# Performance work log

Hardware: AMD Instinct MI355X
Metric: run time of the kernel (lower is better)

## Reference

```python
import jax, jax.numpy as jnp
import numpy as np
import math

DIM = 1024
NUM_HEADS = 16
HEAD_DIM = DIM // NUM_HEADS
LOGIT_SCALE_MAX = math.log(1.0 / 0.01)
EPS = 1e-12  # F.normalize eps


def setup_inputs() -> dict:
    key = jax.random.key(0)
    ks = jax.random.split(key, 4)
    L, N, C = 1024, 8, DIM
    scale = HEAD_DIM ** -0.5
    x = jax.random.normal(ks[0], (L, N, C), dtype=jnp.float32)
    in_proj_weight = jax.random.normal(ks[1], (3 * C, C), dtype=jnp.float32) * scale
    in_proj_bias = jnp.zeros((3 * C,), dtype=jnp.float32)
    logit_scale = jnp.full((NUM_HEADS, 1, 1), math.log(10.0), dtype=jnp.float32)
    head_scale = jnp.ones((NUM_HEADS, 1, 1), dtype=jnp.float32)
    out_w = jax.random.normal(ks[2], (C, C), dtype=jnp.float32) * (C ** -0.5)
    out_b = jax.random.normal(ks[3], (C,), dtype=jnp.float32) * 0.01
    return {"x": x, "in_proj_weight": in_proj_weight, "in_proj_bias": in_proj_bias,
            "logit_scale": logit_scale, "head_scale": head_scale,
            "out_w": out_w, "out_b": out_b}


def _l2_normalize(t):
    # matches F.normalize(t, dim=-1): t / max(||t||_2, eps)
    n = jnp.sqrt(jnp.sum(t * t, axis=-1, keepdims=True))
    return t / jnp.maximum(n, EPS)


def reference(x, in_proj_weight, in_proj_bias, logit_scale, head_scale, out_w, out_b):
    L, N, C = x.shape
    H, hd = NUM_HEADS, HEAD_DIM
    qkv = x @ in_proj_weight.T + in_proj_bias          # (L, N, 3C)
    q, k, v = jnp.split(qkv, 3, axis=-1)               # each (L, N, C)

    def to_heads(t):  # (L, N, C) -> (N, H, L, hd)
        return t.reshape(L, N, H, hd).transpose(1, 2, 0, 3)

    q, k, v = to_heads(q), to_heads(k), to_heads(v)
    # scaled-cosine attention
    ls = jnp.exp(jnp.minimum(logit_scale, LOGIT_SCALE_MAX))  # (H,1,1) broadcasts
    attn = jnp.einsum('nhld,nhmd->nhlm', _l2_normalize(q), _l2_normalize(k)) * ls
    attn = jax.nn.softmax(attn, axis=-1)               # (N, H, L, L)
    o = jnp.einsum('nhlm,nhmd->nhld', attn, v)         # (N, H, L, hd)
    o = o * head_scale                                  # per-head scale
    o = o.transpose(2, 0, 1, 3).reshape(L, N, C)       # back to (L, N, C)
    return o @ out_w.T + out_b
```

## Files before the change

kernel.cpp:

```cpp
#include <hip/hip_runtime.h>
#include <hip/hip_bf16.h>

typedef __hip_bfloat16 bf16;
typedef __attribute__((ext_vector_type(8))) short bf16x8;
typedef __attribute__((ext_vector_type(4))) float f32x4;

#define LOGIT_MAX 4.6051702f

__device__ __forceinline__ float4 load4(const float* p) { return *(const float4*)p; }

__device__ __forceinline__ void store4bf(bf16* p, float4 v) {
    union { bf16 b[4]; uint2 u; } t;
    t.b[0] = __float2bfloat16(v.x); t.b[1] = __float2bfloat16(v.y);
    t.b[2] = __float2bfloat16(v.z); t.b[3] = __float2bfloat16(v.w);
    *(uint2*)p = t.u;
}

__device__ __forceinline__ void async16(const bf16* g, const bf16* lds) {
    __builtin_amdgcn_global_load_lds(
        (const __attribute__((address_space(1))) void*)g,
        (__attribute__((address_space(3))) void*)lds, 16, 0, 0);
}

__global__ __launch_bounds__(256) void prep_kernel(
    const void* __restrict__ x, const void* __restrict__ w_in, const void* __restrict__ out_w,
    const void* __restrict__ b_in, const void* __restrict__ out_b,
    const void* __restrict__ ls, const void* __restrict__ hs,
    bf16* __restrict__ xb, bf16* __restrict__ wb, bf16* __restrict__ owb,
    float* __restrict__ smallf, int* __restrict__ flag)
{
    __shared__ int cnt;
    if (threadIdx.x == 0) cnt = 0;
    __syncthreads();
    {
        const unsigned short* xs = (const unsigned short*)x;
        int c = 0;
        for (int i = threadIdx.x; i < 4096; i += 256) {
            const unsigned e = (xs[i] >> 7) & 0xFF;
            if (e >= 0x90) c++;
        }
        atomicAdd(&cnt, c);
    }
    __syncthreads();
    const int f = (cnt > 64) ? 1 : 0;

    if (blockIdx.x == 0) {
        if (threadIdx.x == 0) *flag = f;
        for (int idx = threadIdx.x; idx < 4128; idx += 256) {
            float v;
            if (f) {
                if (idx < 3072)      v = ((const float*)b_in)[idx];
                else if (idx < 4096) v = ((const float*)out_b)[idx - 3072];
                else if (idx < 4112) v = expf(fminf(((const float*)ls)[idx - 4096], LOGIT_MAX));
                else                 v = ((const float*)hs)[idx - 4112];
            } else {
                if (idx < 3072)      v = __bfloat162float(((const bf16*)b_in)[idx]);
                else if (idx < 4096) v = __bfloat162float(((const bf16*)out_b)[idx - 3072]);
                else if (idx < 4112) v = expf(fminf(__bfloat162float(((const bf16*)ls)[idx - 4096]), LOGIT_MAX));
                else                 v = __bfloat162float(((const bf16*)hs)[idx - 4112]);
            }
            smallf[idx] = v;
        }
    }
    if (f != 1) return;
    const size_t NX = 8388608, NW = 3145728, NO = 1048576;
    const size_t t0   = ((size_t)blockIdx.x * 256 + threadIdx.x) * 4;
    const size_t step = (size_t)gridDim.x * 256 * 4;
    for (size_t i = t0; i < NX; i += step) store4bf(xb + i, load4((const float*)x + i));
    for (size_t i = t0; i < NW; i += step) store4bf(wb + i, load4((const float*)w_in + i));
    for (size_t i = t0; i < NO; i += step) store4bf(owb + i, load4((const float*)out_w + i));
}

__global__ __launch_bounds__(256, 3) void qkv_gemm_mfma_kernel(
    const int* __restrict__ flag,
    const bf16* __restrict__ Xws, const bf16* __restrict__ Wws,
    const bf16* __restrict__ Xdir, const bf16* __restrict__ Wdir,
    const float* __restrict__ bias_f,
    bf16* __restrict__ q, bf16* __restrict__ k, bf16* __restrict__ vt)
{
    const bf16* X = (*flag) ? Xws : Xdir;
    const bf16* W = (*flag) ? Wws : Wdir;
    __shared__ bf16 A_lds[128 * 64];
    __shared__ bf16 B_lds[128 * 64];
    const int tid  = threadIdx.x;
    const int w    = tid >> 6;
    const int lane = tid & 63;
    const int l16  = lane & 15, quad = lane >> 4;
    const int wm   = w >> 1, wn = w & 1;
    const int row0 = blockIdx.y * 128;
    const int col0 = blockIdx.x * 128;
    const int sr   = lane >> 3, sc = lane & 7;
    const int scg  = sc ^ sr;

    f32x4 acc[4][4] = {};

    for (int kt = 0; kt < 1024; kt += 64) {
        __syncthreads();
#pragma unroll
        for (int i = 0; i < 4; i++) {
            const int br = w * 32 + i * 8;
            async16(X + (size_t)(row0 + br + sr) * 1024 + kt + scg * 8, &A_lds[br * 64]);
            async16(W + (size_t)(col0 + br + sr) * 1024 + kt + scg * 8, &B_lds[br * 64]);
        }
        __syncthreads();

#pragma unroll
        for (int kh = 0; kh < 2; kh++) {
            bf16x8 af[4], bf[4];
#pragma unroll
            for (int mt = 0; mt < 4; mt++) {
                const int row = wm * 64 + mt * 16 + l16;
                af[mt] = *(const bf16x8*)&A_lds[row * 64 + (((quad + kh * 4) ^ (row & 7)) * 8)];
            }
#pragma unroll
            for (int nt = 0; nt < 4; nt++) {
                const int row = wn * 64 + nt * 16 + l16;
                bf[nt] = *(const bf16x8*)&B_lds[row * 64 + (((quad + kh * 4) ^ (row & 7)) * 8)];
            }
#pragma unroll
            for (int mt = 0; mt < 4; mt++)
#pragma unroll
                for (int nt = 0; nt < 4; nt++)
                    acc[mt][nt] = __builtin_amdgcn_mfma_f32_16x16x32_bf16(af[mt], bf[nt], acc[mt][nt], 0, 0, 0);
        }
    }

    const int cbase = col0 + wn * 64;
    const int part  = cbase >> 10;
    const int h     = (cbase & 1023) >> 6;
    float bias[4];
#pragma unroll
    for (int nt = 0; nt < 4; nt++) bias[nt] = bias_f[cbase + nt * 16 + l16];

    if (part < 2) {
        bf16* dst0 = (part == 0) ? q : k;
#pragma unroll
        for (int mt = 0; mt < 4; mt++) {
#pragma unroll
            for (int rg = 0; rg < 4; rg++) {
                const int r = row0 + wm * 64 + mt * 16 + quad * 4 + rg;
                const int l = r >> 3, nn = r & 7;
                float val[4]; float ss = 0.f;
#pragma unroll
                for (int nt = 0; nt < 4; nt++) {
                    val[nt] = acc[mt][nt][rg] + bias[nt];
                    ss += val[nt] * val[nt];
                }
                ss += __shfl_xor(ss, 1); ss += __shfl_xor(ss, 2);
                ss += __shfl_xor(ss, 4); ss += __shfl_xor(ss, 8);
                const float inv = 1.f / fmaxf(sqrtf(ss), 1e-12f);
                bf16* dp = dst0 + ((size_t)((nn * 16 + h) * 1024 + l)) * 64;
#pragma unroll
                for (int nt = 0; nt < 4; nt++)
                    dp[nt * 16 + l16] = __float2bfloat16(val[nt] * inv);
            }
        }
    } else {
#pragma unroll
        for (int mt = 0; mt < 4; mt++) {
#pragma unroll
            for (int rg = 0; rg < 4; rg++) {
                const int r = row0 + wm * 64 + mt * 16 + quad * 4 + rg;
                const int l = r >> 3, nn = r & 7;
#pragma unroll
                for (int nt = 0; nt < 4; nt++) {
                    const int d = nt * 16 + l16;
                    vt[((size_t)((nn * 16 + h) * 64 + d)) * 1024 + l] =
                        __float2bfloat16(acc[mt][nt][rg] + bias[nt]);
                }
            }
        }
    }
}

__global__ __launch_bounds__(512, 2) void attn_mfma_kernel(
    const bf16* __restrict__ q, const bf16* __restrict__ k,
    const bf16* __restrict__ vt, const float* __restrict__ scale_f,
    bf16* __restrict__ o)
{
    __shared__ bf16 K_lds[64][64];
    __shared__ bf16 Vt_lds[64][64];
    __shared__ bf16 P_lds[8][32][72];
    __shared__ float l_lds[8][32];

    const int bid  = blockIdx.x;
    const int qt   = bid >> 7;
    const int nh   = bid & 127;
    const int h    = nh & 15;
    const int n    = nh >> 4;
    const int tid  = threadIdx.x;
    const int w    = tid >> 6;
    const int lane = tid & 63;
    const int l16  = lane & 15;
    const int quad = lane >> 4;

    const size_t base = (size_t)nh * (1024 * 64);
    const float ls   = scale_f[4096 + h];
    const float hs   = scale_f[4112 + h];
    const float lsl2 = ls * 1.4426950408889634f;

    bf16x8 qf[2][2];
#pragma unroll
    for (int u = 0; u < 2; u++) {
        const int qrow = qt * 256 + w * 32 + u * 16 + l16;
        const bf16* qp = q + base + (size_t)qrow * 64 + quad * 8;
        qf[u][0] = *(const bf16x8*)qp;
        qf[u][1] = *(const bf16x8*)(qp + 32);
    }

    f32x4 o_acc[2][4] = {};
    float l_part[2] = {0.f, 0.f};

    const int sr = lane >> 3;
    const int sc = lane & 7;

    for (int j0 = 0; j0 < 1024; j0 += 64) {
        __syncthreads();
        {
            const int row = w * 8 + sr;
            const int cg  = sc ^ (row & 7);
            async16(k  + base + (size_t)(j0 + row) * 64 + cg * 8, &K_lds[w * 8][0]);
            async16(vt + base + (size_t)row * 1024 + j0 + cg * 8, &Vt_lds[w * 8][0]);
        }
        __syncthreads();

        f32x4 s8[2][4];
#pragma unroll
        for (int s = 0; s < 4; s++) {
            const int krow = s * 16 + l16;
            const int swz  = krow & 7;
            const bf16x8 kf0 = *(const bf16x8*)&K_lds[krow][(quad ^ swz) * 8];
            const bf16x8 kf1 = *(const bf16x8*)&K_lds[krow][((quad + 4) ^ swz) * 8];
#pragma unroll
            for (int u = 0; u < 2; u++) {
                f32x4 a = {};
                a = __builtin_amdgcn_mfma_f32_16x16x32_bf16(kf0, qf[u][0], a, 0, 0, 0);
                a = __builtin_amdgcn_mfma_f32_16x16x32_bf16(kf1, qf[u][1], a, 0, 0, 0);
                s8[u][s] = a;
            }
        }

#pragma unroll
        for (int u = 0; u < 2; u++) {
#pragma unroll
            for (int s = 0; s < 4; s++) {
                union { bf16 b[4]; uint2 uu; } pk;
                float sum = 0.f;
#pragma unroll
                for (int r = 0; r < 4; r++) {
                    const float p = exp2f(fmaf(s8[u][s][r], lsl2, -lsl2));
                    pk.b[r] = __float2bfloat16(p);
                    sum += p;
                }
                l_part[u] += sum;
                *(uint2*)&P_lds[w][u * 16 + l16][s * 16 + quad * 4] = pk.uu;
            }
        }

        bf16x8 pf[2][2];
#pragma unroll
        for (int u = 0; u < 2; u++) {
            pf[u][0] = *(const bf16x8*)&P_lds[w][u * 16 + l16][quad * 8];
            pf[u][1] = *(const bf16x8*)&P_lds[w][u * 16 + l16][32 + quad * 8];
        }
#pragma unroll
        for (int ds = 0; ds < 4; ds++) {
            const int vrow = ds * 16 + l16;
            const int swz  = vrow & 7;
            const bf16x8 vf0 = *(const bf16x8*)&Vt_lds[vrow][(quad ^ swz) * 8];
            const bf16x8 vf1 = *(const bf16x8*)&Vt_lds[vrow][((quad + 4) ^ swz) * 8];
#pragma unroll
            for (int u = 0; u < 2; u++) {
                o_acc[u][ds] = __builtin_amdgcn_mfma_f32_16x16x32_bf16(pf[u][0], vf0, o_acc[u][ds], 0, 0, 0);
                o_acc[u][ds] = __builtin_amdgcn_mfma_f32_16x16x32_bf16(pf[u][1], vf1, o_acc[u][ds], 0, 0, 0);
            }
        }
    }

#pragma unroll
    for (int u = 0; u < 2; u++) {
        float v = l_part[u];
        v += __shfl_xor(v, 16);
        v += __shfl_xor(v, 32);
        l_lds[w][u * 16 + l16] = v;
    }

#pragma unroll
    for (int u = 0; u < 2; u++) {
#pragma unroll
        for (int r = 0; r < 4; r++) {
            const float inv = hs / l_lds[w][u * 16 + quad * 4 + r];
            const int row_l = qt * 256 + w * 32 + u * 16 + quad * 4 + r;
            bf16* dst = o + ((size_t)row_l * 8 + n) * 1024 + h * 64 + l16;
#pragma unroll
            for (int ds = 0; ds < 4; ds++)
                dst[ds * 16] = __float2bfloat16(o_acc[u][ds][r] * inv);
        }
    }
}

__global__ __launch_bounds__(256, 3) void out_gemm_mfma_kernel(
    const int* __restrict__ flag,
    const bf16* __restrict__ A,
    const bf16* __restrict__ Bws, const bf16* __restrict__ Bdir,
    const float* __restrict__ bias_f,
    float* __restrict__ outf, bf16* __restrict__ outb)
{
    const int f = *flag;
    const bf16* B = f ? Bws : Bdir;
    __shared__ bf16 A_lds[128 * 64];
    __shared__ bf16 B_lds[128 * 64];
    const int tid  = threadIdx.x;
    const int w    = tid >> 6;
    const int lane = tid & 63;
    const int l16  = lane & 15, quad = lane >> 4;
    const int wm   = w >> 1, wn = w & 1;
    const int row0 = blockIdx.y * 128;
    const int col0 = blockIdx.x * 128;
    const int sr   = lane >> 3, sc = lane & 7;
    const int scg  = sc ^ sr;

    f32x4 acc[4][4] = {};

    for (int kt = 0; kt < 1024; kt += 64) {
        __syncthreads();
#pragma unroll
        for (int i = 0; i < 4; i++) {
            const int br = w * 32 + i * 8;
            async16(A + (size_t)(row0 + br + sr) * 1024 + kt + scg * 8, &A_lds[br * 64]);
            async16(B + (size_t)(col0 + br + sr) * 1024 + kt + scg * 8, &B_lds[br * 64]);
        }
        __syncthreads();

#pragma unroll
        for (int kh = 0; kh < 2; kh++) {
            bf16x8 af[4], bf[4];
#pragma unroll
            for (int mt = 0; mt < 4; mt++) {
                const int row = wm * 64 + mt * 16 + l16;
                af[mt] = *(const bf16x8*)&A_lds[row * 64 + (((quad + kh * 4) ^ (row & 7)) * 8)];
            }
#pragma unroll
            for (int nt = 0; nt < 4; nt++) {
                const int row = wn * 64 + nt * 16 + l16;
                bf[nt] = *(const bf16x8*)&B_lds[row * 64 + (((quad + kh * 4) ^ (row & 7)) * 8)];
            }
#pragma unroll
            for (int mt = 0; mt < 4; mt++)
#pragma unroll
                for (int nt = 0; nt < 4; nt++)
                    acc[mt][nt] = __builtin_amdgcn_mfma_f32_16x16x32_bf16(af[mt], bf[nt], acc[mt][nt], 0, 0, 0);
        }
    }

#pragma unroll
    for (int mt = 0; mt < 4; mt++) {
        const int rbase = row0 + wm * 64 + mt * 16 + quad * 4;
#pragma unroll
        for (int nt = 0; nt < 4; nt++) {
            const int c = col0 + wn * 64 + nt * 16 + l16;
            const float bias = bias_f[c];
#pragma unroll
            for (int rg = 0; rg < 4; rg++) {
                const float v = acc[mt][nt][rg] + bias;
                const size_t idx = (size_t)(rbase + rg) * 1024 + c;
                if (f) outf[idx] = v; else outb[idx] = __float2bfloat16(v);
            }
        }
    }
}

extern "C" void kernel_launch(void* const* d_in, const int* in_sizes, int n_in,
                              void* d_out, int out_size, void* d_ws, size_t ws_size,
                              hipStream_t stream)
{
    const size_t SEG = (size_t)8 * 16 * 1024 * 64;
    bf16* qn  = (bf16*)d_ws;
    bf16* kn  = qn + SEG;
    bf16* vt  = kn + SEG;
    bf16* ow  = vt + SEG;
    bf16* xb  = ow + SEG;
    bf16* wb  = xb + SEG;
    bf16* owb = wb + 3145728;
    float* smallf = (float*)(owb + 1048576);
    int*   flag   = (int*)(smallf + 4128);

    prep_kernel<<<4096, 256, 0, stream>>>(
        d_in[0], d_in[1], d_in[5], d_in[2], d_in[6], d_in[3], d_in[4],
        xb, wb, owb, smallf, flag);

    qkv_gemm_mfma_kernel<<<dim3(3072 / 128, 8192 / 128), 256, 0, stream>>>(
        flag, xb, wb, (const bf16*)d_in[0], (const bf16*)d_in[1], smallf, qn, kn, vt);

    attn_mfma_kernel<<<dim3(128 * 4), 512, 0, stream>>>(qn, kn, vt, smallf, ow);

    out_gemm_mfma_kernel<<<dim3(1024 / 128, 8192 / 128), 256, 0, stream>>>(
        flag, ow, owb, (const bf16*)d_in[5], smallf + 3072,
        (float*)d_out, (bf16*)d_out);
}
```

Baseline: 288.0 us.

## Fuse all stages into one persistent cooperative kernel with grid syncs

Replaces the four kernel launches (prep, QKV GEMM, attention, output GEMM) with one cooperative kernel that walks each stage's tiles in grid-stride fashion and separates stages with grid.sync. The attention stage now uses 256-thread blocks covering 128 queries instead of 512 threads covering 256, and the grid is capped at 512 blocks based on occupancy. This is meant to remove launch gaps and tail effects between kernels, at the cost of grid-wide barriers, a fixed persistent grid, shared-memory reuse across stages, and possibly lower per-stage occupancy.

```diff
diff --git a/kernel.cpp b/kernel.cpp
--- a/kernel.cpp
+++ b/kernel.cpp
@@ -1,5 +1,8 @@
 #include <hip/hip_runtime.h>
+#include <hip/hip_cooperative_groups.h>
 #include <hip/hip_bf16.h>
+
+namespace cg = cooperative_groups;
 
 typedef __hip_bfloat16 bf16;
 typedef __attribute__((ext_vector_type(8))) short bf16x8;
@@ -22,20 +25,32 @@
         (__attribute__((address_space(3))) void*)lds, 16, 0, 0);
 }
 
-__global__ __launch_bounds__(256) void prep_kernel(
+__global__ __launch_bounds__(256, 2) void fused_kernel(
     const void* __restrict__ x, const void* __restrict__ w_in, const void* __restrict__ out_w,
     const void* __restrict__ b_in, const void* __restrict__ out_b,
     const void* __restrict__ ls, const void* __restrict__ hs,
     bf16* __restrict__ xb, bf16* __restrict__ wb, bf16* __restrict__ owb,
-    float* __restrict__ smallf, int* __restrict__ flag)
+    float* __restrict__ smallf,
+    bf16* __restrict__ qn, bf16* __restrict__ kn, bf16* __restrict__ vtb,
+    bf16* __restrict__ ow, void* __restrict__ outp)
 {
+    __shared__ __align__(16) char shraw[35328];
     __shared__ int cnt;
-    if (threadIdx.x == 0) cnt = 0;
+    cg::grid_group grid = cg::this_grid();
+
+    const int tid  = threadIdx.x;
+    const int bid  = blockIdx.x;
+    const int nblk = gridDim.x;
+    const int w    = tid >> 6;
+    const int lane = tid & 63;
+    const int l16  = lane & 15, quad = lane >> 4;
+
+    if (tid == 0) cnt = 0;
     __syncthreads();
     {
         const unsigned short* xs = (const unsigned short*)x;
         int c = 0;
-        for (int i = threadIdx.x; i < 4096; i += 256) {
+        for (int i = tid; i < 4096; i += 256) {
             const unsigned e = (xs[i] >> 7) & 0xFF;
             if (e >= 0x90) c++;
         }
@@ -44,9 +59,8 @@
     __syncthreads();
     const int f = (cnt > 64) ? 1 : 0;
 
-    if (blockIdx.x == 0) {
-        if (threadIdx.x == 0) *flag = f;
-        for (int idx = threadIdx.x; idx < 4128; idx += 256) {
+    if (bid == 0) {
+        for (int idx = tid; idx < 4128; idx += 256) {
             float v;
             if (f) {
                 if (idx < 3072)      v = ((const float*)b_in)[idx];
@@ -62,309 +76,299 @@
             smallf[idx] = v;
         }
     }
-    if (f != 1) return;
-    const size_t NX = 8388608, NW = 3145728, NO = 1048576;
-    const size_t t0   = ((size_t)blockIdx.x * 256 + threadIdx.x) * 4;
-    const size_t step = (size_t)gridDim.x * 256 * 4;
-    for (size_t i = t0; i < NX; i += step) store4bf(xb + i, load4((const float*)x + i));
-    for (size_t i = t0; i < NW; i += step) store4bf(wb + i, load4((const float*)w_in + i));
-    for (size_t i = t0; i < NO; i += step) store4bf(owb + i, load4((const float*)out_w + i));
-}
-
-__global__ __launch_bounds__(256, 3) void qkv_gemm_mfma_kernel(
-    const int* __restrict__ flag,
-    const bf16* __restrict__ Xws, const bf16* __restrict__ Wws,
-    const bf16* __restrict__ Xdir, const bf16* __restrict__ Wdir,
-    const float* __restrict__ bias_f,
-    bf16* __restrict__ q, bf16* __restrict__ k, bf16* __restrict__ vt)
-{
-    const bf16* X = (*flag) ? Xws : Xdir;
-    const bf16* W = (*flag) ? Wws : Wdir;
-    __shared__ bf16 A_lds[128 * 64];
-    __shared__ bf16 B_lds[128 * 64];
-    const int tid  = threadIdx.x;
-    const int w    = tid >> 6;
-    const int lane = tid & 63;
-    const int l16  = lane & 15, quad = lane >> 4;
-    const int wm   = w >> 1, wn = w & 1;
-    const int row0 = blockIdx.y * 128;
-    const int col0 = blockIdx.x * 128;
-    const int sr   = lane >> 3, sc = lane & 7;
-    const int scg  = sc ^ sr;
-
-    f32x4 acc[4][4] = {};
-
-    for (int kt = 0; kt < 1024; kt += 64) {
-        __syncthreads();
-#pragma unroll
-        for (int i = 0; i < 4; i++) {
-            const int br = w * 32 + i * 8;
-            async16(X + (size_t)(row0 + br + sr) * 1024 + kt + scg * 8, &A_lds[br * 64]);
-            async16(W + (size_t)(col0 + br + sr) * 1024 + kt + scg * 8, &B_lds[br * 64]);
+    if (f) {
+        const size_t NX = 8388608, NW = 3145728, NO = 1048576;
+        const size_t t0   = ((size_t)bid * 256 + tid) * 4;
+        const size_t step = (size_t)nblk * 256 * 4;
+        for (size_t i = t0; i < NX; i += step) store4bf(xb + i, load4((const float*)x + i));
+        for (size_t i = t0; i < NW; i += step) store4bf(wb + i, load4((const float*)w_in + i));
+        for (size_t i = t0; i < NO; i += step) store4bf(owb + i, load4((const float*)out_w + i));
+    }
+    grid.sync();
+
+    {
+        const bf16* X = f ? xb : (const bf16*)x;
+        const bf16* W = f ? wb : (const bf16*)w_in;
+        bf16* A_lds = (bf16*)shraw;
+        bf16* B_lds = (bf16*)shraw + 8192;
+        const float* bias_f = smallf;
+        const int wm = w >> 1, wn = w & 1;
+        const int sr = lane >> 3, sc = lane & 7;
+        const int scg = sc ^ sr;
+
+        for (int t = bid; t < 1536; t += nblk) {
+            const int bx = t % 24, by = t / 24;
+            const int row0 = by * 128;
+            const int col0 = bx * 128;
+
+            f32x4 acc[4][4] = {};
+
+            for (int kt = 0; kt < 1024; kt += 64) {
+                __syncthreads();
+#pragma unroll
+                for (int i = 0; i < 4; i++) {
+                    const int br = w * 32 + i * 8;
+                    async16(X + (size_t)(row0 + br + sr) * 1024 + kt + scg * 8, &A_lds[br * 64]);
+                    async16(W + (size_t)(col0 + br + sr) * 1024 + kt + scg * 8, &B_lds[br * 64]);
+                }
+                __syncthreads();
+
+#pragma unroll
+                for (int kh = 0; kh < 2; kh++) {
+                    bf16x8 af[4], bfr[4];
+#pragma unroll
+                    for (int mt = 0; mt < 4; mt++) {
+                        const int row = wm * 64 + mt * 16 + l16;
+                        af[mt] = *(const bf16x8*)&A_lds[row * 64 + (((quad + kh * 4) ^ (row & 7)) * 8)];
+                    }
+#pragma unroll
+                    for (int nt = 0; nt < 4; nt++) {
+                        const int row = wn * 64 + nt * 16 + l16;
+                        bfr[nt] = *(const bf16x8*)&B_lds[row * 64 + (((quad + kh * 4) ^ (row & 7)) * 8)];
+                    }
+#pragma unroll
+                    for (int mt = 0; mt < 4; mt++)
+#pragma unroll
+                        for (int nt = 0; nt < 4; nt++)
+                            acc[mt][nt] = __builtin_amdgcn_mfma_f32_16x16x32_bf16(af[mt], bfr[nt], acc[mt][nt], 0, 0, 0);
+                }
+            }
+
+            const int cbase = col0 + wn * 64;
+            const int part  = cbase >> 10;
+            const int h     = (cbase & 1023) >> 6;
+            float bias[4];
+#pragma unroll
+            for (int nt = 0; nt < 4; nt++) bias[nt] = bias_f[cbase + nt * 16 + l16];
+
+            if (part < 2) {
+                bf16* dst0 = (part == 0) ? qn : kn;
+#pragma unroll
+                for (int mt = 0; mt < 4; mt++) {
+#pragma unroll
+                    for (int rg = 0; rg < 4; rg++) {
+                        const int r = row0 + wm * 64 + mt * 16 + quad * 4 + rg;
+                        const int l = r >> 3, nn = r & 7;
+                        float val[4]; float ss = 0.f;
+#pragma unroll
+                        for (int nt = 0; nt < 4; nt++) {
+                            val[nt] = acc[mt][nt][rg] + bias[nt];
+                            ss += val[nt] * val[nt];
+                        }
+                        ss += __shfl_xor(ss, 1); ss += __shfl_xor(ss, 2);
+                        ss += __shfl_xor(ss, 4); ss += __shfl_xor(ss, 8);
+                        const float inv = 1.f / fmaxf(sqrtf(ss), 1e-12f);
+                        bf16* dp = dst0 + ((size_t)((nn * 16 + h) * 1024 + l)) * 64;
+#pragma unroll
+                        for (int nt = 0; nt < 4; nt++)
+                            dp[nt * 16 + l16] = __float2bfloat16(val[nt] * inv);
+                    }
+                }
+            } else {
+#pragma unroll
+                for (int mt = 0; mt < 4; mt++) {
+#pragma unroll
+                    for (int rg = 0; rg < 4; rg++) {
+                        const int r = row0 + wm * 64 + mt * 16 + quad * 4 + rg;
+                        const int l = r >> 3, nn = r & 7;
+#pragma unroll
+                        for (int nt = 0; nt < 4; nt++) {
+                            const int d = nt * 16 + l16;
+                            vtb[((size_t)((nn * 16 + h) * 64 + d)) * 1024 + l] =
+                                __float2bfloat16(acc[mt][nt][rg] + bias[nt]);
+                        }
+                    }
+                }
+            }
         }
-        __syncthreads();
-
-#pragma unroll
-        for (int kh = 0; kh < 2; kh++) {
-            bf16x8 af[4], bf[4];
+    }
+    grid.sync();
+
+    {
+        bf16 (*K_lds)[64]      = (bf16 (*)[64])shraw;
+        bf16 (*Vt_lds)[64]     = (bf16 (*)[64])(shraw + 8192);
+        bf16 (*P_lds)[32][72]  = (bf16 (*)[32][72])(shraw + 16384);
+        float (*l_lds)[32]     = (float (*)[32])(shraw + 34816);
+        const float* scale_f   = smallf;
+
+        for (int uu = bid; uu < 1024; uu += nblk) {
+            const int qt = uu >> 7;
+            const int nh = uu & 127;
+            const int h  = nh & 15;
+            const int n  = nh >> 4;
+
+            const size_t base = (size_t)nh * (1024 * 64);
+            const float lsv  = scale_f[4096 + h];
+            const float hsv  = scale_f[4112 + h];
+            const float lsl2 = lsv * 1.4426950408889634f;
+
+            bf16x8 qf[2][2];
+#pragma unroll
+            for (int u = 0; u < 2; u++) {
+                const int qrow = qt * 128 + w * 32 + u * 16 + l16;
+                const bf16* qp = qn + base + (size_t)qrow * 64 + quad * 8;
+                qf[u][0] = *(const bf16x8*)qp;
+                qf[u][1] = *(const bf16x8*)(qp + 32);
+            }
+
+            f32x4 o_acc[2][4] = {};
+            float l_part[2] = {0.f, 0.f};
+
+            const int sr = lane >> 3;
+            const int sc = lane & 7;
+
+            for (int j0 = 0; j0 < 1024; j0 += 64) {
+                __syncthreads();
+#pragma unroll
+                for (int half = 0; half < 2; half++) {
+                    const int br  = w * 16 + half * 8;
+                    const int row = br + sr;
+                    const int cg  = sc ^ (row & 7);
+                    async16(kn  + base + (size_t)(j0 + row) * 64 + cg * 8, &K_lds[br][0]);
+                    async16(vtb + base + (size_t)row * 1024 + j0 + cg * 8, &Vt_lds[br][0]);
+                }
+                __syncthreads();
+
+                f32x4 s8[2][4];
+#pragma unroll
+                for (int s = 0; s < 4; s++) {
+                    const int krow = s * 16 + l16;
+                    const int swz  = krow & 7;
+                    const bf16x8 kf0 = *(const bf16x8*)&K_lds[krow][(quad ^ swz) * 8];
+                    const bf16x8 kf1 = *(const bf16x8*)&K_lds[krow][((quad + 4) ^ swz) * 8];
+#pragma unroll
+                    for (int u = 0; u < 2; u++) {
+                        f32x4 a = {};
+                        a = __builtin_amdgcn_mfma_f32_16x16x32_bf16(kf0, qf[u][0], a, 0, 0, 0);
+                        a = __builtin_amdgcn_mfma_f32_16x16x32_bf16(kf1, qf[u][1], a, 0, 0, 0);
+                        s8[u][s] = a;
+                    }
+                }
+
+#pragma unroll
+                for (int u = 0; u < 2; u++) {
+#pragma unroll
+                    for (int s = 0; s < 4; s++) {
+                        union { bf16 b[4]; uint2 uu2; } pk;
+                        float sum = 0.f;
+#pragma unroll
+                        for (int r = 0; r < 4; r++) {
+                            const float p = exp2f(fmaf(s8[u][s][r], lsl2, -lsl2));
+                            pk.b[r] = __float2bfloat16(p);
+                            sum += p;
+                        }
+                        l_part[u] += sum;
+                        *(uint2*)&P_lds[w][u * 16 + l16][s * 16 + quad * 4] = pk.uu2;
+                    }
+                }
+
+                bf16x8 pf[2][2];
+#pragma unroll
+                for (int u = 0; u < 2; u++) {
+                    pf[u][0] = *(const bf16x8*)&P_lds[w][u * 16 + l16][quad * 8];
+                    pf[u][1] = *(const bf16x8*)&P_lds[w][u * 16 + l16][32 + quad * 8];
+                }
+#pragma unroll
+                for (int ds = 0; ds < 4; ds++) {
+                    const int vrow = ds * 16 + l16;
+                    const int swz  = vrow & 7;
+                    const bf16x8 vf0 = *(const bf16x8*)&Vt_lds[vrow][(quad ^ swz) * 8];
+                    const bf16x8 vf1 = *(const bf16x8*)&Vt_lds[vrow][((quad + 4) ^ swz) * 8];
+#pragma unroll
+                    for (int u = 0; u < 2; u++) {
+                        o_acc[u][ds] = __builtin_amdgcn_mfma_f32_16x16x32_bf16(pf[u][0], vf0, o_acc[u][ds], 0, 0, 0);
+                        o_acc[u][ds] = __builtin_amdgcn_mfma_f32_16x16x32_bf16(pf[u][1], vf1, o_acc[u][ds], 0, 0, 0);
+                    }
+                }
+            }
+
+#pragma unroll
+            for (int u = 0; u < 2; u++) {
+                float v = l_part[u];
+                v += __shfl_xor(v, 16);
+                v += __shfl_xor(v, 32);
+                l_lds[w][u * 16 + l16] = v;
+            }
+
+#pragma unroll
+            for (int u = 0; u < 2; u++) {
+#pragma unroll
+                for (int r = 0; r < 4; r++) {
+                    const float inv = hsv / l_lds[w][u * 16 + quad * 4 + r];
+                    const int row_l = qt * 128 + w * 32 + u * 16 + quad * 4 + r;
+                    bf16* dst = ow + ((size_t)row_l * 8 + n) * 1024 + h * 64 + l16;
+#pragma unroll
+                    for (int ds = 0; ds < 4; ds++)
+                        dst[ds * 16] = __float2bfloat16(o_acc[u][ds][r] * inv);
+                }
+            }
+        }
+    }
+    grid.sync();
+
+    {
+        const bf16* B = f ? owb : (const bf16*)out_w;
+        bf16* A_lds = (bf16*)shraw;
+        bf16* B_lds = (bf16*)shraw + 8192;
+        const float* bias_f = smallf + 3072;
+        float* outf = (float*)outp;
+        bf16*  outb = (bf16*)outp;
+        const int wm = w >> 1, wn = w & 1;
+        const int sr = lane >> 3, sc = lane & 7;
+        const int scg = sc ^ sr;
+
+        for (int t = bid; t < 512; t += nblk) {
+            const int bx = t & 7, by = t >> 3;
+            const int row0 = by * 128;
+            const int col0 = bx * 128;
+
+            f32x4 acc[4][4] = {};
+
+            for (int kt = 0; kt < 1024; kt += 64) {
+                __syncthreads();
+#pragma unroll
+                for (int i = 0; i < 4; i++) {
+                    const int br = w * 32 + i * 8;
+                    async16(ow + (size_t)(row0 + br + sr) * 1024 + kt + scg * 8, &A_lds[br * 64]);
+                    async16(B  + (size_t)(col0 + br + sr) * 1024 + kt + scg * 8, &B_lds[br * 64]);
+                }
+                __syncthreads();
+
+#pragma unroll
+                for (int kh = 0; kh < 2; kh++) {
+                    bf16x8 af[4], bfr[4];
+#pragma unroll
+                    for (int mt = 0; mt < 4; mt++) {
+                        const int row = wm * 64 + mt * 16 + l16;
+                        af[mt] = *(const bf16x8*)&A_lds[row * 64 + (((quad + kh * 4) ^ (row & 7)) * 8)];
+                    }
+#pragma unroll
+                    for (int nt = 0; nt < 4; nt++) {
+                        const int row = wn * 64 + nt * 16 + l16;
+                        bfr[nt] = *(const bf16x8*)&B_lds[row * 64 + (((quad + kh * 4) ^ (row & 7)) * 8)];
+                    }
+#pragma unroll
+                    for (int mt = 0; mt < 4; mt++)
+#pragma unroll
+                        for (int nt = 0; nt < 4; nt++)
+                            acc[mt][nt] = __builtin_amdgcn_mfma_f32_16x16x32_bf16(af[mt], bfr[nt], acc[mt][nt], 0, 0, 0);
+                }
+            }
+
 #pragma unroll
             for (int mt = 0; mt < 4; mt++) {
-                const int row = wm * 64 + mt * 16 + l16;
-                af[mt] = *(const bf16x8*)&A_lds[row * 64 + (((quad + kh * 4) ^ (row & 7)) * 8)];
-            }
-#pragma unroll
-            for (int nt = 0; nt < 4; nt++) {
-                const int row = wn * 64 + nt * 16 + l16;
-                bf[nt] = *(const bf16x8*)&B_lds[row * 64 + (((quad + kh * 4) ^ (row & 7)) * 8)];
-            }
-#pragma unroll
-            for (int mt = 0; mt < 4; mt++)
-#pragma unroll
-                for (int nt = 0; nt < 4; nt++)
-                    acc[mt][nt] = __builtin_amdgcn_mfma_f32_16x16x32_bf16(af[mt], bf[nt], acc[mt][nt], 0, 0, 0);
-        }
-    }
-
-    const int cbase = col0 + wn * 64;
-    const int part  = cbase >> 10;
-    const int h     = (cbase & 1023) >> 6;
-    float bias[4];
-#pragma unroll
-    for (int nt = 0; nt < 4; nt++) bias[nt] = bias_f[cbase + nt * 16 + l16];
-
-    if (part < 2) {
-        bf16* dst0 = (part == 0) ? q : k;
-#pragma unroll
-        for (int mt = 0; mt < 4; mt++) {
-#pragma unroll
-            for (int rg = 0; rg < 4; rg++) {
-                const int r = row0 + wm * 64 + mt * 16 + quad * 4 + rg;
-                const int l = r >> 3, nn = r & 7;
-                float val[4]; float ss = 0.f;
+                const int rbase = row0 + wm * 64 + mt * 16 + quad * 4;
 #pragma unroll
                 for (int nt = 0; nt < 4; nt++) {
-                    val[nt] = acc[mt][nt][rg] + bias[nt];
-                    ss += val[nt] * val[nt];
-                }
-                ss += __shfl_xor(ss, 1); ss += __shfl_xor(ss, 2);
-                ss += __shfl_xor(ss, 4); ss += __shfl_xor(ss, 8);
-                const float inv = 1.f / fmaxf(sqrtf(ss), 1e-12f);
-                bf16* dp = dst0 + ((size_t)((nn * 16 + h) * 1024 + l)) * 64;
-#pragma unroll
-                for (int nt = 0; nt < 4; nt++)
-                    dp[nt * 16 + l16] = __float2bfloat16(val[nt] * inv);
-            }
-        }
-    } else {
-#pragma unroll
-        for (int mt = 0; mt < 4; mt++) {
-#pragma unroll
-            for (int rg = 0; rg < 4; rg++) {
-                const int r = row0 + wm * 64 + mt * 16 + quad * 4 + rg;
-                const int l = r >> 3, nn = r & 7;
-#pragma unroll
-                for (int nt = 0; nt < 4; nt++) {
-                    const int d = nt * 16 + l16;
-                    vt[((size_t)((nn * 16 + h) * 64 + d)) * 1024 + l] =
-                        __float2bfloat16(acc[mt][nt][rg] + bias[nt]);
-                }
-            }
-        }
-    }
-}
-
-__global__ __launch_bounds__(512, 2) void attn_mfma_kernel(
-    const bf16* __restrict__ q, const bf16* __restrict__ k,
-    const bf16* __restrict__ vt, const float* __restrict__ scale_f,
-    bf16* __restrict__ o)
-{
-    __shared__ bf16 K_lds[64][64];
-    __shared__ bf16 Vt_lds[64][64];
-    __shared__ bf16 P_lds[8][32][72];
-    __shared__ float l_lds[8][32];
-
-    const int bid  = blockIdx.x;
-    const int qt   = bid >> 7;
-    const int nh   = bid & 127;
-    const int h    = nh & 15;
-    const int n    = nh >> 4;
-    const int tid  = threadIdx.x;
-    const int w    = tid >> 6;
-    const int lane = tid & 63;
-    const int l16  = lane & 15;
-    const int quad = lane >> 4;
-
-    const size_t base = (size_t)nh * (1024 * 64);
-    const float ls   = scale_f[4096 + h];
-    const float hs   = scale_f[4112 + h];
-    const float lsl2 = ls * 1.4426950408889634f;
-
-    bf16x8 qf[2][2];
-#pragma unroll
-    for (int u = 0; u < 2; u++) {
-        const int qrow = qt * 256 + w * 32 + u * 16 + l16;
-        const bf16* qp = q + base + (size_t)qrow * 64 + quad * 8;
-        qf[u][0] = *(const bf16x8*)qp;
-        qf[u][1] = *(const bf16x8*)(qp + 32);
-    }
-
-    f32x4 o_acc[2][4] = {};
-    float l_part[2] = {0.f, 0.f};
-
-    const int sr = lane >> 3;
-    const int sc = lane & 7;
-
-    for (int j0 = 0; j0 < 1024; j0 += 64) {
-        __syncthreads();
-        {
-            const int row = w * 8 + sr;
-            const int cg  = sc ^ (row & 7);
-            async16(k  + base + (size_t)(j0 + row) * 64 + cg * 8, &K_lds[w * 8][0]);
-            async16(vt + base + (size_t)row * 1024 + j0 + cg * 8, &Vt_lds[w * 8][0]);
-        }
-        __syncthreads();
-
-        f32x4 s8[2][4];
-#pragma unroll
-        for (int s = 0; s < 4; s++) {
-            const int krow = s * 16 + l16;
-            const int swz  = krow & 7;
-            const bf16x8 kf0 = *(const bf16x8*)&K_lds[krow][(quad ^ swz) * 8];
-            const bf16x8 kf1 = *(const bf16x8*)&K_lds[krow][((quad + 4) ^ swz) * 8];
-#pragma unroll
-            for (int u = 0; u < 2; u++) {
-                f32x4 a = {};
-                a = __builtin_amdgcn_mfma_f32_16x16x32_bf16(kf0, qf[u][0], a, 0, 0, 0);
-                a = __builtin_amdgcn_mfma_f32_16x16x32_bf16(kf1, qf[u][1], a, 0, 0, 0);
-                s8[u][s] = a;
-            }
-        }
-
-#pragma unroll
-        for (int u = 0; u < 2; u++) {
-#pragma unroll
-            for (int s = 0; s < 4; s++) {
-                union { bf16 b[4]; uint2 uu; } pk;
-                float sum = 0.f;
-#pragma unroll
-                for (int r = 0; r < 4; r++) {
-                    const float p = exp2f(fmaf(s8[u][s][r], lsl2, -lsl2));
-                    pk.b[r] = __float2bfloat16(p);
-                    sum += p;
-                }
-                l_part[u] += sum;
-                *(uint2*)&P_lds[w][u * 16 + l16][s * 16 + quad * 4] = pk.uu;
-            }
-        }
-
-        bf16x8 pf[2][2];
-#pragma unroll
-        for (int u = 0; u < 2; u++) {
-            pf[u][0] = *(const bf16x8*)&P_lds[w][u * 16 + l16][quad * 8];
-            pf[u][1] = *(const bf16x8*)&P_lds[w][u * 16 + l16][32 + quad * 8];
-        }
-#pragma unroll
-        for (int ds = 0; ds < 4; ds++) {
-            const int vrow = ds * 16 + l16;
-            const int swz  = vrow & 7;
-            const bf16x8 vf0 = *(const bf16x8*)&Vt_lds[vrow][(quad ^ swz) * 8];
-            const bf16x8 vf1 = *(const bf16x8*)&Vt_lds[vrow][((quad + 4) ^ swz) * 8];
-#pragma unroll
-            for (int u = 0; u < 2; u++) {
-                o_acc[u][ds] = __builtin_amdgcn_mfma_f32_16x16x32_bf16(pf[u][0], vf0, o_acc[u][ds], 0, 0, 0);
-                o_acc[u][ds] = __builtin_amdgcn_mfma_f32_16x16x32_bf16(pf[u][1], vf1, o_acc[u][ds], 0, 0, 0);
-            }
-        }
-    }
-
-#pragma unroll
-    for (int u = 0; u < 2; u++) {
-        float v = l_part[u];
-        v += __shfl_xor(v, 16);
-        v += __shfl_xor(v, 32);
-        l_lds[w][u * 16 + l16] = v;
-    }
-
-#pragma unroll
-    for (int u = 0; u < 2; u++) {
-#pragma unroll
-        for (int r = 0; r < 4; r++) {
-            const float inv = hs / l_lds[w][u * 16 + quad * 4 + r];
-            const int row_l = qt * 256 + w * 32 + u * 16 + quad * 4 + r;
-            bf16* dst = o + ((size_t)row_l * 8 + n) * 1024 + h * 64 + l16;
-#pragma unroll
-            for (int ds = 0; ds < 4; ds++)
-                dst[ds * 16] = __float2bfloat16(o_acc[u][ds][r] * inv);
-        }
-    }
-}
-
-__global__ __launch_bounds__(256, 3) void out_gemm_mfma_kernel(
-    const int* __restrict__ flag,
-    const bf16* __restrict__ A,
-    const bf16* __restrict__ Bws, const bf16* __restrict__ Bdir,
-    const float* __restrict__ bias_f,
-    float* __restrict__ outf, bf16* __restrict__ outb)
-{
-    const int f = *flag;
-    const bf16* B = f ? Bws : Bdir;
-    __shared__ bf16 A_lds[128 * 64];
-    __shared__ bf16 B_lds[128 * 64];
-    const int tid  = threadIdx.x;
-    const int w    = tid >> 6;
-    const int lane = tid & 63;
-    const int l16  = lane & 15, quad = lane >> 4;
-    const int wm   = w >> 1, wn = w & 1;
-    const int row0 = blockIdx.y * 128;
-    const int col0 = blockIdx.x * 128;
-    const int sr   = lane >> 3, sc = lane & 7;
-    const int scg  = sc ^ sr;
-
-    f32x4 acc[4][4] = {};
-
-    for (int kt = 0; kt < 1024; kt += 64) {
-        __syncthreads();
-#pragma unroll
-        for (int i = 0; i < 4; i++) {
-            const int br = w * 32 + i * 8;
-            async16(A + (size_t)(row0 + br + sr) * 1024 + kt + scg * 8, &A_lds[br * 64]);
-            async16(B + (size_t)(col0 + br + sr) * 1024 + kt + scg * 8, &B_lds[br * 64]);
-        }
-        __syncthreads();
-
-#pragma unroll
-        for (int kh = 0; kh < 2; kh++) {
-            bf16x8 af[4], bf[4];
-#pragma unroll
-            for (int mt = 0; mt < 4; mt++) {
-                const int row = wm * 64 + mt * 16 + l16;
-                af[mt] = *(const bf16x8*)&A_lds[row * 64 + (((quad + kh * 4) ^ (row & 7)) * 8)];
-            }
-#pragma unroll
-            for (int nt = 0; nt < 4; nt++) {
-                const int row = wn * 64 + nt * 16 + l16;
-                bf[nt] = *(const bf16x8*)&B_lds[row * 64 + (((quad + kh * 4) ^ (row & 7)) * 8)];
-            }
-#pragma unroll
-            for (int mt = 0; mt < 4; mt++)
-#pragma unroll
-                for (int nt = 0; nt < 4; nt++)
-                    acc[mt][nt] = __builtin_amdgcn_mfma_f32_16x16x32_bf16(af[mt], bf[nt], acc[mt][nt], 0, 0, 0);
-        }
-    }
-
-#pragma unroll
-    for (int mt = 0; mt < 4; mt++) {
-        const int rbase = row0 + wm * 64 + mt * 16 + quad * 4;
-#pragma unroll
-        for (int nt = 0; nt < 4; nt++) {
-            const int c = col0 + wn * 64 + nt * 16 + l16;
-            const float bias = bias_f[c];
-#pragma unroll
-            for (int rg = 0; rg < 4; rg++) {
-                const float v = acc[mt][nt][rg] + bias;
-                const size_t idx = (size_t)(rbase + rg) * 1024 + c;
-                if (f) outf[idx] = v; else outb[idx] = __float2bfloat16(v);
+                    const int c = col0 + wn * 64 + nt * 16 + l16;
+                    const float bias = bias_f[c];
+#pragma unroll
+                    for (int rg = 0; rg < 4; rg++) {
+                        const float v = acc[mt][nt][rg] + bias;
+                        const size_t idx = (size_t)(rbase + rg) * 1024 + c;
+                        if (f) outf[idx] = v; else outb[idx] = __float2bfloat16(v);
+                    }
+                }
             }
         }
     }
@@ -383,18 +387,33 @@
     bf16* wb  = xb + SEG;
     bf16* owb = wb + 3145728;
     float* smallf = (float*)(owb + 1048576);
-    int*   flag   = (int*)(smallf + 4128);
-
-    prep_kernel<<<4096, 256, 0, stream>>>(
-        d_in[0], d_in[1], d_in[5], d_in[2], d_in[6], d_in[3], d_in[4],
-        xb, wb, owb, smallf, flag);
-
-    qkv_gemm_mfma_kernel<<<dim3(3072 / 128, 8192 / 128), 256, 0, stream>>>(
-        flag, xb, wb, (const bf16*)d_in[0], (const bf16*)d_in[1], smallf, qn, kn, vt);
-
-    attn_mfma_kernel<<<dim3(128 * 4), 512, 0, stream>>>(qn, kn, vt, smallf, ow);
-
-    out_gemm_mfma_kernel<<<dim3(1024 / 128, 8192 / 128), 256, 0, stream>>>(
-        flag, ow, owb, (const bf16*)d_in[5], smallf + 3072,
-        (float*)d_out, (bf16*)d_out);
+
+    static int g_grid = 0;
+    if (g_grid == 0) {
+        int nb = 0;
+        if (hipOccupancyMaxActiveBlocksPerMultiprocessor(&nb, (const void*)fused_kernel, 256, 0) != hipSuccess || nb < 1)
+            nb = 1;
+        int g = nb * 256;
+        if (g > 512) g = 512;
+        g_grid = g;
+    }
+
+    const void* x_  = d_in[0];
+    const void* w_  = d_in[1];
+    const void* owt = d_in[5];
+    const void* bi_ = d_in[2];
+    const void* bo_ = d_in[6];
+    const void* ls_ = d_in[3];
+    const void* hs_ = d_in[4];
+    void* out_ = d_out;
+
+    void* kargs[] = {
+        (void*)&x_, (void*)&w_, (void*)&owt, (void*)&bi_, (void*)&bo_,
+        (void*)&ls_, (void*)&hs_,
+        (void*)&xb, (void*)&wb, (void*)&owb, (void*)&smallf,
+        (void*)&qn, (void*)&kn, (void*)&vt, (void*)&ow, (void*)&out_
+    };
+
+    hipLaunchCooperativeKernel((const void*)fused_kernel,
+                               dim3(g_grid), dim3(256), kargs, 0, stream);
 }
```

New measurement: 507.0 us. +76.0%, slower.
